# Performance work log

Measured on AMD Instinct MI355X. Metric: run time of the kernel, lower is better.

Reference implementation:

```python
import jax, jax.numpy as jnp
import numpy as np

# Static graph / model sizes (closed over; match input_specs)
N0, N1, N2 = 500_000, 100_000, 25_000   # nodes per hop (targets are prefix of sources)
E0, E1 = 1_600_000, 400_000             # edges per hop
D_IN, D_H, D_OUT = 128, 256, 128


def setup_inputs() -> dict:
    key = jax.random.key(0)
    ks = jax.random.split(key, 11)
    s_in = 1.0 / np.sqrt(D_IN)
    s_h = 1.0 / np.sqrt(D_H)
    return {
        "x": jax.random.normal(ks[0], (N0, D_IN), dtype=jnp.float32),
        # layer 0 params (SAGEConv in->hidden): lin_l (with bias) on aggregated, lin_r (no bias) on root
        "W_l0": jax.random.normal(ks[1], (D_H, D_IN), dtype=jnp.float32) * s_in,
        "b_l0": jax.random.normal(ks[2], (D_H,), dtype=jnp.float32) * s_in,
        "W_r0": jax.random.normal(ks[3], (D_H, D_IN), dtype=jnp.float32) * s_in,
        # layer 1 params (SAGEConv hidden->out)
        "W_l1": jax.random.normal(ks[4], (D_OUT, D_H), dtype=jnp.float32) * s_h,
        "b_l1": jax.random.normal(ks[5], (D_OUT,), dtype=jnp.float32) * s_h,
        "W_r1": jax.random.normal(ks[6], (D_OUT, D_H), dtype=jnp.float32) * s_h,
        # bipartite edge indices: src in [0, N_src), dst in [0, N_dst)
        "ei0_src": jax.random.randint(ks[7], (E0,), 0, N0),
        "ei0_dst": jax.random.randint(ks[8], (E0,), 0, N1),
        "ei1_src": jax.random.randint(ks[9], (E1,), 0, N1),
        "ei1_dst": jax.random.randint(ks[10], (E1,), 0, N2),
    }


def _sage_conv(x_src, x_dst, src, dst, n_dst, W_l, b_l, W_r):
    """PyG SAGEConv, aggr='mean': lin_l(mean_neigh) + lin_r(x_dst)."""
    msg = x_src[src]                                                # [E, d] gather
    agg = jax.ops.segment_sum(msg, dst, num_segments=n_dst)        # [n_dst, d]
    cnt = jax.ops.segment_sum(jnp.ones((src.shape[0],), msg.dtype), dst,
                              num_segments=n_dst)                  # [n_dst]
    agg = agg / jnp.clip(cnt, 1.0)[:, None]                        # mean (safe for isolated nodes)
    return agg @ W_l.T + b_l + x_dst @ W_r.T


def reference(x, W_l0, b_l0, W_r0, W_l1, b_l1, W_r1,
              ei0_src, ei0_dst, ei1_src, ei1_dst):
    # hop 0: targets are first N1 rows of x
    h = _sage_conv(x, x[:N1], ei0_src, ei0_dst, N1, W_l0, b_l0, W_r0)
    h = jax.nn.relu(h)  # relu on all but last layer
    # hop 1 (last layer, no relu)
    out = _sage_conv(h, h[:N2], ei1_src, ei1_dst, N2, W_l1, b_l1, W_r1)
    return out
```

## Files before the change

### kernel.cpp

```cpp
#include <hip/hip_runtime.h>
#include <hip/hip_bf16.h>

#define cN0 500000
#define cN1 100000
#define cN2 25000
#define cE0 1600000
#define cE1 400000

typedef __bf16 bf16x8 __attribute__((ext_vector_type(8)));
typedef __bf16 bf16x4 __attribute__((ext_vector_type(4)));
typedef float f32x4 __attribute__((ext_vector_type(4)));


__global__ void k_hist(const int* __restrict__ d0, const int* __restrict__ d1,
                       int* __restrict__ c0, int* __restrict__ c1) {
    int i = blockIdx.x * blockDim.x + threadIdx.x;
    if (i < cE0) {
        atomicAdd(&c0[d0[i]], 1);
    } else {
        int j = i - cE0;
        if (j < cE1) atomicAdd(&c1[d1[j]], 1);
    }
}

__global__ void k_scan1(int* __restrict__ a0, int* __restrict__ a1, int nb0,
                        int* __restrict__ bsum) {
    __shared__ int lds[256];
    const int t = threadIdx.x;
    int* a; int n; int* bs; int bb;
    if ((int)blockIdx.x < nb0) { a = a0; n = cN1; bs = bsum;       bb = blockIdx.x; }
    else                       { a = a1; n = cN2; bs = bsum + 128; bb = blockIdx.x - nb0; }
    const int base = bb * 1024 + t * 4;
    int v0 = (base + 0 < n) ? a[base + 0] : 0;
    int v1 = (base + 1 < n) ? a[base + 1] : 0;
    int v2 = (base + 2 < n) ? a[base + 2] : 0;
    int v3 = (base + 3 < n) ? a[base + 3] : 0;
    const int s = v0 + v1 + v2 + v3;
    lds[t] = s;
    __syncthreads();
    int x = s;
    for (int d = 1; d < 256; d <<= 1) {
        int y = (t >= d) ? lds[t - d] : 0;
        __syncthreads();
        x += y;
        lds[t] = x;
        __syncthreads();
    }
    if (t == 255) bs[bb] = x;
    int e0 = x - s;
    int e1 = e0 + v0, e2 = e1 + v1, e3 = e2 + v2;
    if (base + 0 < n) a[base + 0] = e0;
    if (base + 1 < n) a[base + 1] = e1;
    if (base + 2 < n) a[base + 2] = e2;
    if (base + 3 < n) a[base + 3] = e3;
}

__global__ void k_scan2(int* __restrict__ bsum, int nb0, int nb1) {
    __shared__ int lds[128];
    const int t = threadIdx.x;
    int* bs = bsum + blockIdx.x * 128;
    const int nb = (blockIdx.x == 0) ? nb0 : nb1;
    int v = (t < nb) ? bs[t] : 0;
    lds[t] = v;
    __syncthreads();
    int x = v;
    for (int d = 1; d < 128; d <<= 1) {
        int y = (t >= d) ? lds[t - d] : 0;
        __syncthreads();
        x += y;
        lds[t] = x;
        __syncthreads();
    }
    if (t < nb) bs[t] = x - v;
}

__global__ void k_scan3(int* __restrict__ off0, int* __restrict__ off1,
                        const int* __restrict__ bsum,
                        int* __restrict__ cur0, int* __restrict__ cur1) {
    int i = blockIdx.x * blockDim.x + threadIdx.x;
    if (i < cN1) {
        int v = off0[i] + bsum[i >> 10];
        off0[i] = v;
        cur0[i] = v;
    }
    if (i < cN2) {
        int v = off1[i] + bsum[128 + (i >> 10)];
        off1[i] = v;
        cur1[i] = v;
    }
    if (i == 0) { off0[cN1] = cE0; off1[cN2] = cE1; }
}

__global__ void k_scatter(const int* __restrict__ e0s, const int* __restrict__ e0d,
                          const int* __restrict__ e1s, const int* __restrict__ e1d,
                          int* __restrict__ cur0, int* __restrict__ cur1,
                          int* __restrict__ srcs0, int* __restrict__ srcs1) {
    int i = blockIdx.x * blockDim.x + threadIdx.x;
    if (i < cE0) {
        int p = atomicAdd(&cur0[e0d[i]], 1);
        srcs0[p] = e0s[i];
    } else {
        int j = i - cE0;
        if (j < cE1) {
            int p = atomicAdd(&cur1[e1d[j]], 1);
            srcs1[p] = e1s[j];
        }
    }
}

__global__ void k_wcat(const float* __restrict__ Wl0, const float* __restrict__ Wr0,
                       const float* __restrict__ Wl1, const float* __restrict__ Wr1,
                       __bf16* __restrict__ Wc0, __bf16* __restrict__ Wc1) {
    int i = blockIdx.x * blockDim.x + threadIdx.x;
    if (i < 256 * 256) {
        int j = i >> 8, k = i & 255;
        float v = (k < 128) ? Wl0[j * 128 + k] : Wr0[j * 128 + (k - 128)];
        Wc0[i] = (__bf16)v;
    } else {
        int i2 = i - 256 * 256;
        if (i2 < 128 * 512) {
            int j = i2 >> 9, k = i2 & 511;
            float v = (k < 256) ? Wl1[j * 256 + k] : Wr1[j * 256 + (k - 256)];
            Wc1[i2] = (__bf16)v;
        }
    }
}

__global__ __launch_bounds__(256) void k_cast(const float* __restrict__ x,
                                              __bf16* __restrict__ xb,
                                              __bf16* __restrict__ M0) {
    const size_t t = (size_t)blockIdx.x * 256 + threadIdx.x;
    const size_t base = t * 8;
    const f32x4 a = __builtin_nontemporal_load((const f32x4*)(x + base));
    const f32x4 b = __builtin_nontemporal_load((const f32x4*)(x + base + 4));
    bf16x8 o;
    o[0] = (__bf16)a[0]; o[1] = (__bf16)a[1]; o[2] = (__bf16)a[2]; o[3] = (__bf16)a[3];
    o[4] = (__bf16)b[0]; o[5] = (__bf16)b[1]; o[6] = (__bf16)b[2]; o[7] = (__bf16)b[3];
    *(bf16x8*)(xb + base) = o;
    const int row = (int)(base >> 7);
    if (row < cN1) {
        const int col = (int)(base & 127);
        *(bf16x8*)(M0 + (size_t)row * 256 + 128 + col) = o;
    }
}

__global__ __launch_bounds__(256) void k_agg0(
    const __bf16* __restrict__ xb,
    const int* __restrict__ off, const int* __restrict__ srcs,
    __bf16* __restrict__ M0)
{
    const int tid = threadIdx.x;
    const int slot = tid >> 5;
    const int ln = tid & 31;
    const int g = blockIdx.x * 8 + slot;
    if (g >= cN1) return;
    const int e0 = off[g], e1 = off[g + 1];
    float a0 = 0.f, a1 = 0.f, a2 = 0.f, a3 = 0.f;
    int e = e0;
    for (; e + 4 <= e1; e += 4) {
        const int s0 = srcs[e], s1 = srcs[e + 1], s2 = srcs[e + 2], s3 = srcs[e + 3];
        const bf16x4 r0 = *(const bf16x4*)(xb + (size_t)s0 * 128 + ln * 4);
        const bf16x4 r1 = *(const bf16x4*)(xb + (size_t)s1 * 128 + ln * 4);
        const bf16x4 r2 = *(const bf16x4*)(xb + (size_t)s2 * 128 + ln * 4);
        const bf16x4 r3 = *(const bf16x4*)(xb + (size_t)s3 * 128 + ln * 4);
        a0 += ((float)r0[0] + (float)r1[0]) + ((float)r2[0] + (float)r3[0]);
        a1 += ((float)r0[1] + (float)r1[1]) + ((float)r2[1] + (float)r3[1]);
        a2 += ((float)r0[2] + (float)r1[2]) + ((float)r2[2] + (float)r3[2]);
        a3 += ((float)r0[3] + (float)r1[3]) + ((float)r2[3] + (float)r3[3]);
    }
    for (; e < e1; ++e) {
        const int s = srcs[e];
        const bf16x4 r = *(const bf16x4*)(xb + (size_t)s * 128 + ln * 4);
        a0 += (float)r[0]; a1 += (float)r[1]; a2 += (float)r[2]; a3 += (float)r[3];
    }
    const int cnt = e1 - e0;
    const float inv = 1.f / (float)(cnt > 0 ? cnt : 1);
    bf16x4 oa;
    oa[0] = (__bf16)(a0 * inv); oa[1] = (__bf16)(a1 * inv);
    oa[2] = (__bf16)(a2 * inv); oa[3] = (__bf16)(a3 * inv);
    *(bf16x4*)(M0 + (size_t)g * 256 + ln * 4) = oa;
}

__global__ __launch_bounds__(256) void k_agg1(
    const __bf16* __restrict__ h,
    const int* __restrict__ off, const int* __restrict__ srcs,
    __bf16* __restrict__ M1)
{
    const int tid = threadIdx.x;
    const int wave = tid >> 6;
    const int lane = tid & 63;
    const int g = blockIdx.x * 4 + wave;
    if (g >= cN2) return;
    const int e0 = off[g], e1 = off[g + 1];
    float a0 = 0.f, a1 = 0.f, a2 = 0.f, a3 = 0.f;
    int e = e0;
    for (; e + 4 <= e1; e += 4) {
        const int s0 = srcs[e], s1 = srcs[e + 1], s2 = srcs[e + 2], s3 = srcs[e + 3];
        const bf16x4 r0 = *(const bf16x4*)(h + (size_t)s0 * 256 + lane * 4);
        const bf16x4 r1 = *(const bf16x4*)(h + (size_t)s1 * 256 + lane * 4);
        const bf16x4 r2 = *(const bf16x4*)(h + (size_t)s2 * 256 + lane * 4);
        const bf16x4 r3 = *(const bf16x4*)(h + (size_t)s3 * 256 + lane * 4);
        a0 += (float)r0[0] + (float)r1[0] + (float)r2[0] + (float)r3[0];
        a1 += (float)r0[1] + (float)r1[1] + (float)r2[1] + (float)r3[1];
        a2 += (float)r0[2] + (float)r1[2] + (float)r2[2] + (float)r3[2];
        a3 += (float)r0[3] + (float)r1[3] + (float)r2[3] + (float)r3[3];
    }
    for (; e < e1; ++e) {
        const int s = srcs[e];
        const bf16x4 r = *(const bf16x4*)(h + (size_t)s * 256 + lane * 4);
        a0 += (float)r[0]; a1 += (float)r[1]; a2 += (float)r[2]; a3 += (float)r[3];
    }
    const int cnt = e1 - e0;
    const float inv = 1.f / (float)(cnt > 0 ? cnt : 1);
    bf16x4 oa;
    oa[0] = (__bf16)(a0 * inv); oa[1] = (__bf16)(a1 * inv);
    oa[2] = (__bf16)(a2 * inv); oa[3] = (__bf16)(a3 * inv);
    *(bf16x4*)(M1 + (size_t)g * 512 + lane * 4) = oa;
    *(bf16x4*)(M1 + (size_t)g * 512 + 256 + lane * 4) =
        *(const bf16x4*)(h + (size_t)g * 256 + lane * 4);
}

template<int K, int LDC, int NJ, int UNR, bool RELU, bool OUTBF16>
__global__ __launch_bounds__(256) void k_gemm(
    const __bf16* __restrict__ Mm, const __bf16* __restrict__ W,
    const float* __restrict__ bias,
    float* __restrict__ outf, __bf16* __restrict__ outb, int Mrows)
{
    const int tid = threadIdx.x;
    const int l = tid & 63;
    const int w = tid >> 6;
    const int wm = w & 1, wn = w >> 1;
    const int row0 = blockIdx.x * 128 + wm * 64;
    const int col0 = blockIdx.y * (NJ * 32) + wn * (NJ * 16);
    const int lr = l & 15;
    const int lk = (l >> 4) * 8;

    const __bf16* pa[4];
    const __bf16* pb[NJ];
    #pragma unroll
    for (int i = 0; i < 4; ++i) {
        int r = row0 + i * 16 + lr;
        r = (r < Mrows) ? r : (Mrows - 1);
        pa[i] = Mm + (size_t)r * K + lk;
    }
    #pragma unroll
    for (int j = 0; j < NJ; ++j)
        pb[j] = W + (size_t)(col0 + j * 16 + lr) * K + lk;

    f32x4 acc[4][NJ];
    #pragma unroll
    for (int i = 0; i < 4; ++i)
        #pragma unroll
        for (int j = 0; j < NJ; ++j)
            acc[i][j] = (f32x4)0.0f;

    #pragma unroll UNR
    for (int k0 = 0; k0 < K; k0 += 32) {
        bf16x8 fa[4], fb[NJ];
        #pragma unroll
        for (int i = 0; i < 4; ++i) fa[i] = *(const bf16x8*)(pa[i] + k0);
        #pragma unroll
        for (int j = 0; j < NJ; ++j) fb[j] = *(const bf16x8*)(pb[j] + k0);
        #pragma unroll
        for (int i = 0; i < 4; ++i)
            #pragma unroll
            for (int j = 0; j < NJ; ++j)
                acc[i][j] = __builtin_amdgcn_mfma_f32_16x16x32_bf16(fa[i], fb[j], acc[i][j], 0, 0, 0);
    }

    #pragma unroll
    for (int j = 0; j < NJ; ++j) {
        const int colg = col0 + j * 16 + lr;
        const float bj = bias[colg];
        #pragma unroll
        for (int i = 0; i < 4; ++i) {
            #pragma unroll
            for (int reg = 0; reg < 4; ++reg) {
                const int rowg = row0 + i * 16 + (l >> 4) * 4 + reg;
                if (rowg < Mrows) {
                    float v = acc[i][j][reg] + bj;
                    if (RELU) v = fmaxf(v, 0.f);
                    if (OUTBF16) outb[(size_t)rowg * LDC + colg] = (__bf16)v;
                    else         outf[(size_t)rowg * LDC + colg] = v;
                }
            }
        }
    }
}


extern "C" void kernel_launch(void* const* d_in, const int* in_sizes, int n_in,
                              void* d_out, int out_size, void* d_ws, size_t ws_size,
                              hipStream_t stream) {
    const float* x   = (const float*)d_in[0];
    const float* Wl0 = (const float*)d_in[1];
    const float* bl0 = (const float*)d_in[2];
    const float* Wr0 = (const float*)d_in[3];
    const float* Wl1 = (const float*)d_in[4];
    const float* bl1 = (const float*)d_in[5];
    const float* Wr1 = (const float*)d_in[6];
    const int* e0s = (const int*)d_in[7];
    const int* e0d = (const int*)d_in[8];
    const int* e1s = (const int*)d_in[9];
    const int* e1d = (const int*)d_in[10];
    float* out = (float*)d_out;

    char* ws = (char*)d_ws;
    size_t pos = 0;
    auto alloc = [&](size_t nb) -> void* {
        void* p = ws + pos;
        pos += (nb + 255) & ~(size_t)255;
        return p;
    };
    __bf16* xb   = (__bf16*)alloc((size_t)cN0 * 128 * 2);
    __bf16* h    = xb;
    __bf16* M0   = (__bf16*)alloc((size_t)cN1 * 256 * 2);
    __bf16* M1   = M0;
    int* off0    = (int*)alloc((size_t)(cN1 + 1 + cN2 + 1) * 4);
    int* off1    = off0 + (cN1 + 1);
    int* cur0    = (int*)alloc((size_t)cN1 * 4);
    int* cur1    = (int*)alloc((size_t)cN2 * 4);
    int* srcs0   = (int*)alloc((size_t)cE0 * 4);
    int* srcs1   = (int*)alloc((size_t)cE1 * 4);
    int* bsum    = (int*)alloc(256 * 4);
    __bf16* Wc0  = (__bf16*)alloc(256 * 256 * 2);
    __bf16* Wc1  = (__bf16*)alloc(128 * 512 * 2);
    (void)ws_size; (void)in_sizes; (void)n_in; (void)out_size;

    const int nb0 = (cN1 + 1023) / 1024;
    const int nb1 = (cN2 + 1023) / 1024;

    hipMemsetAsync(off0, 0, (size_t)(cN1 + 1 + cN2 + 1) * 4, stream);
    k_hist<<<(cE0 + cE1 + 255) / 256, 256, 0, stream>>>(e0d, e1d, off0, off1);
    k_scan1<<<nb0 + nb1, 256, 0, stream>>>(off0, off1, nb0, bsum);
    k_scan2<<<2, 128, 0, stream>>>(bsum, nb0, nb1);
    k_scan3<<<(cN1 + 255) / 256, 256, 0, stream>>>(off0, off1, bsum, cur0, cur1);
    k_scatter<<<(cE0 + cE1 + 255) / 256, 256, 0, stream>>>(e0s, e0d, e1s, e1d,
                                                           cur0, cur1, srcs0, srcs1);

    k_wcat<<<(256 * 256 + 128 * 512 + 255) / 256, 256, 0, stream>>>(Wl0, Wr0, Wl1, Wr1, Wc0, Wc1);

    k_cast<<<(cN0 * 128 / 8) / 256, 256, 0, stream>>>(x, xb, M0);

    k_agg0<<<(cN1 + 7) / 8, 256, 0, stream>>>(xb, off0, srcs0, M0);
    {
        dim3 grid((cN1 + 127) / 128, 1);
        k_gemm<256, 256, 8, 1, true, true><<<grid, 256, 0, stream>>>(M0, Wc0, bl0, nullptr, h, cN1);
    }
    k_agg1<<<(cN2 + 3) / 4, 256, 0, stream>>>(h, off1, srcs1, M1);
    {
        dim3 grid((cN2 + 127) / 128, 1);
        k_gemm<512, 128, 4, 2, false, false><<<grid, 256, 0, stream>>>(M1, Wc1, bl1, out, nullptr, cN2);
    }
}
```

Measured before the change: 871.8 us.

## Partition histogram and scatter atomics by destination range; split layer-0 GEMM over columns

The histogram and CSR scatter kernels now use 4096 blocks. Each block strides over the edge list but only handles destinations in one of 8 contiguous ranges, so each range's atomics stay within a smaller, more cache-resident slice of counters. The price is that every edge index is read 8 times. Separately, the layer-0 GEMM grid gains a second dimension with different template parameters, splitting output columns across two blocks to get more parallelism.

```diff
diff --git a/kernel.cpp b/kernel.cpp
--- a/kernel.cpp
+++ b/kernel.cpp
@@ -11,15 +11,17 @@
 typedef __bf16 bf16x4 __attribute__((ext_vector_type(4)));
 typedef float f32x4 __attribute__((ext_vector_type(4)));
 
-
-__global__ void k_hist(const int* __restrict__ d0, const int* __restrict__ d1,
-                       int* __restrict__ c0, int* __restrict__ c1) {
-    int i = blockIdx.x * blockDim.x + threadIdx.x;
-    if (i < cE0) {
-        atomicAdd(&c0[d0[i]], 1);
-    } else {
-        int j = i - cE0;
-        if (j < cE1) atomicAdd(&c1[d1[j]], 1);
+__global__ void k_histx(const int* __restrict__ d0, const int* __restrict__ d1,
+                        int* __restrict__ c0, int* __restrict__ c1) {
+    int b = blockIdx.x;
+    const int* d; int* c; int E, sz;
+    if (b < 2048) { d = d0; c = c0; E = cE0; sz = 12500; }
+    else          { b -= 2048; d = d1; c = c1; E = cE1; sz = 3125; }
+    const int lo = (b & 7) * sz, hi = lo + sz;
+    int i = (b >> 3) * 256 + threadIdx.x;
+    for (; i < E; i += 65536) {
+        const int dv = d[i];
+        if (dv >= lo && dv < hi) atomicAdd(&c[dv], 1);
     }
 }
 
@@ -91,19 +93,21 @@
     if (i == 0) { off0[cN1] = cE0; off1[cN2] = cE1; }
 }
 
-__global__ void k_scatter(const int* __restrict__ e0s, const int* __restrict__ e0d,
-                          const int* __restrict__ e1s, const int* __restrict__ e1d,
-                          int* __restrict__ cur0, int* __restrict__ cur1,
-                          int* __restrict__ srcs0, int* __restrict__ srcs1) {
-    int i = blockIdx.x * blockDim.x + threadIdx.x;
-    if (i < cE0) {
-        int p = atomicAdd(&cur0[e0d[i]], 1);
-        srcs0[p] = e0s[i];
-    } else {
-        int j = i - cE0;
-        if (j < cE1) {
-            int p = atomicAdd(&cur1[e1d[j]], 1);
-            srcs1[p] = e1s[j];
+__global__ void k_scatx(const int* __restrict__ s0, const int* __restrict__ d0,
+                        const int* __restrict__ s1, const int* __restrict__ d1,
+                        int* __restrict__ cur0, int* __restrict__ cur1,
+                        int* __restrict__ o0, int* __restrict__ o1) {
+    int b = blockIdx.x;
+    const int *s, *d; int *cur, *o; int E, sz;
+    if (b < 2048) { s = s0; d = d0; cur = cur0; o = o0; E = cE0; sz = 12500; }
+    else          { b -= 2048; s = s1; d = d1; cur = cur1; o = o1; E = cE1; sz = 3125; }
+    const int lo = (b & 7) * sz, hi = lo + sz;
+    int i = (b >> 3) * 256 + threadIdx.x;
+    for (; i < E; i += 65536) {
+        const int dv = d[i];
+        if (dv >= lo && dv < hi) {
+            const int p = atomicAdd(&cur[dv], 1);
+            o[p] = s[i];
         }
     }
 }
@@ -331,12 +335,11 @@
     const int nb1 = (cN2 + 1023) / 1024;
 
     hipMemsetAsync(off0, 0, (size_t)(cN1 + 1 + cN2 + 1) * 4, stream);
-    k_hist<<<(cE0 + cE1 + 255) / 256, 256, 0, stream>>>(e0d, e1d, off0, off1);
+    k_histx<<<4096, 256, 0, stream>>>(e0d, e1d, off0, off1);
     k_scan1<<<nb0 + nb1, 256, 0, stream>>>(off0, off1, nb0, bsum);
     k_scan2<<<2, 128, 0, stream>>>(bsum, nb0, nb1);
     k_scan3<<<(cN1 + 255) / 256, 256, 0, stream>>>(off0, off1, bsum, cur0, cur1);
-    k_scatter<<<(cE0 + cE1 + 255) / 256, 256, 0, stream>>>(e0s, e0d, e1s, e1d,
-                                                           cur0, cur1, srcs0, srcs1);
+    k_scatx<<<4096, 256, 0, stream>>>(e0s, e0d, e1s, e1d, cur0, cur1, srcs0, srcs1);
 
     k_wcat<<<(256 * 256 + 128 * 512 + 255) / 256, 256, 0, stream>>>(Wl0, Wr0, Wl1, Wr1, Wc0, Wc1);
 
@@ -344,8 +347,8 @@
 
     k_agg0<<<(cN1 + 7) / 8, 256, 0, stream>>>(xb, off0, srcs0, M0);
     {
-        dim3 grid((cN1 + 127) / 128, 1);
-        k_gemm<256, 256, 8, 1, true, true><<<grid, 256, 0, stream>>>(M0, Wc0, bl0, nullptr, h, cN1);
+        dim3 grid((cN1 + 127) / 128, 2);
+        k_gemm<256, 256, 4, 2, true, true><<<grid, 256, 0, stream>>>(M0, Wc0, bl0, nullptr, h, cN1);
     }
     k_agg1<<<(cN2 + 3) / 4, 256, 0, stream>>>(h, off1, srcs1, M1);
     {
```

Result: faster. 745.9 us (-14.4%).
